# Optimization experiments

Hardware: AMD Instinct MI355X
Metric: run time of the kernel (lower is better)

## Reference

```python
import jax, jax.numpy as jnp
import numpy as np

B, N, K = 4, 40960, 16
D_IN, D_OUT = 32, 64


def setup_inputs() -> dict:
    key = jax.random.key(0)
    keys = iter(jax.random.split(key, 48))
    def nrm(shape, scale):
        return (jax.random.normal(next(keys), shape, jnp.float32) * scale).astype(jnp.float32)
    inp = {
        "feature": jax.random.normal(next(keys), (B, N, D_IN), jnp.float32),
        "xyz": jax.random.uniform(next(keys), (B, N, 3), jnp.float32),
        "neigh_idx": jax.random.randint(next(keys), (B, N, K), 0, N, jnp.int32),
    }
    def conv_bn(name, cin, cout):
        inp["w_" + name] = nrm((cin, cout), (2.0 / cin) ** 0.5)
        inp["s_" + name] = 1.0 + nrm((cout,), 0.1)  # folded BN scale: gamma/sqrt(var+eps)
        inp["b_" + name] = nrm((cout,), 0.1)        # folded BN bias: beta - mean*scale
    conv_bn("mlp1", D_IN, D_OUT // 2)
    conv_bn("lfa1", 10, D_OUT // 2)
    inp["w_att1_fc"] = nrm((D_OUT, D_OUT), (2.0 / D_OUT) ** 0.5)
    conv_bn("att1_mlp", D_OUT, D_OUT // 2)
    conv_bn("lfa2", D_OUT // 2, D_OUT // 2)
    inp["w_att2_fc"] = nrm((D_OUT, D_OUT), (2.0 / D_OUT) ** 0.5)
    conv_bn("att2_mlp", D_OUT, D_OUT)
    conv_bn("mlp2", D_OUT, 2 * D_OUT)
    conv_bn("sc", D_IN, 2 * D_OUT)
    return inp


def _gather(pc, idx):
    # pc: [B,N,D], idx: [B,N,K] -> [B,N,K,D]
    b, n, k = idx.shape
    flat = jnp.take_along_axis(pc, idx.reshape(b, n * k, 1), axis=1)
    return flat.reshape(b, n, k, pc.shape[-1])


def _cb(x, w, s, b, relu=True):
    # 1x1 conv + folded BN (+ ReLU), channels-last
    y = jnp.einsum('...i,io->...o', x, w) * s + b
    return jnp.maximum(y, 0.0) if relu else y


def _att_pool(fs, w_fc, w, s, b):
    # fs: [B,N,K,C]; softmax-attention pooling over K, then mlp
    scores = jax.nn.softmax(jnp.einsum('bnkc,cd->bnkd', fs, w_fc), axis=2)
    agg = jnp.sum(fs * scores, axis=2)  # [B,N,C]
    return _cb(agg, w, s, b)


def _rel_pos(xyz, idx):
    nbr = _gather(xyz, idx)                           # [B,N,K,3]
    tile = jnp.broadcast_to(xyz[:, :, None, :], nbr.shape)
    rel = tile - nbr
    dist = jnp.sqrt(jnp.sum(rel * rel, axis=-1, keepdims=True))
    return jnp.concatenate([dist, rel, tile, nbr], axis=-1)  # [B,N,K,10]


def reference(feature, xyz, neigh_idx,
              w_mlp1, s_mlp1, b_mlp1,
              w_lfa1, s_lfa1, b_lfa1,
              w_att1_fc, w_att1_mlp, s_att1_mlp, b_att1_mlp,
              w_lfa2, s_lfa2, b_lfa2,
              w_att2_fc, w_att2_mlp, s_att2_mlp, b_att2_mlp,
              w_mlp2, s_mlp2, b_mlp2,
              w_sc, s_sc, b_sc):
    f_pc = _cb(feature, w_mlp1, s_mlp1, b_mlp1)                   # [B,N,d/2]
    f_xyz = _cb(_rel_pos(xyz, neigh_idx), w_lfa1, s_lfa1, b_lfa1)  # [B,N,K,d/2]
    f_nb = _gather(f_pc, neigh_idx)                                # [B,N,K,d/2]
    f_agg = _att_pool(jnp.concatenate([f_nb, f_xyz], axis=-1),
                      w_att1_fc, w_att1_mlp, s_att1_mlp, b_att1_mlp)  # [B,N,d/2]
    f_xyz2 = _cb(f_xyz, w_lfa2, s_lfa2, b_lfa2)                    # [B,N,K,d/2]
    f_nb2 = _gather(f_agg, neigh_idx)                              # [B,N,K,d/2]
    f_pc2 = _att_pool(jnp.concatenate([f_nb2, f_xyz2], axis=-1),
                      w_att2_fc, w_att2_mlp, s_att2_mlp, b_att2_mlp)  # [B,N,d]
    out = _cb(f_pc2, w_mlp2, s_mlp2, b_mlp2, relu=False)           # [B,N,2d]
    sc = _cb(feature, w_sc, s_sc, b_sc, relu=False)
    return jax.nn.leaky_relu(out + sc, negative_slope=0.2)
```

## Files before the change

### kernel.cpp

```cpp
#include <hip/hip_runtime.h>
#include <hip/hip_bf16.h>

#define NPTS  40960
#define BNPTS 163840
#define KNB   16

#define PK_MLP1 0
#define PK_FC1  1280
#define PK_FC2  6912
#define PK_L1   12544
#define PK_L2   13824
#define PK_M1   15104
#define PK_M2   17920
#define PK_W2   23552
#define PK_WS   34816
#define PK_TOTAL 39936

using bf16x8 = __attribute__((ext_vector_type(8))) short;
using f32x4  = __attribute__((ext_vector_type(4))) float;

__device__ __forceinline__ unsigned short f2bf(float x) {
    union { float f; unsigned u; } v; v.f = x;
    unsigned r = v.u + 0x7fffu + ((v.u >> 16) & 1u);
    return (unsigned short)(r >> 16);
}
__device__ __forceinline__ float bf2f(unsigned short u) {
    union { unsigned u; float f; } v; v.u = ((unsigned)u) << 16;
    return v.f;
}
__device__ __forceinline__ unsigned pk2(float lo, float hi) {
    union { __hip_bfloat162 h; unsigned u; } v;
    v.h = __float22bfloat162_rn(float2{lo, hi});
    return v.u;
}
__device__ __forceinline__ bf16x8 pack8(float a0, float a1, float a2, float a3,
                                        float a4, float a5, float a6, float a7) {
    union { unsigned u[4]; bf16x8 v; } w;
    w.u[0] = pk2(a0, a1); w.u[1] = pk2(a2, a3);
    w.u[2] = pk2(a4, a5); w.u[3] = pk2(a6, a7);
    return w.v;
}
__device__ __forceinline__ f32x4 mfma16(bf16x8 a, bf16x8 b, f32x4 c) {
    return __builtin_amdgcn_mfma_f32_16x16x32_bf16(a, b, c, 0, 0, 0);
}
__device__ __forceinline__ float exp2_fast(float x) { return __builtin_amdgcn_exp2f(x); }
__device__ __forceinline__ float rcp_fast(float x)  { return __builtin_amdgcn_rcpf(x); }

__global__ __launch_bounds__(256)
void k_prep(const float* __restrict__ wm1, const float* __restrict__ wfc1,
            const float* __restrict__ wfc2,
            const float* __restrict__ wlfa1, const float* __restrict__ slfa1, const float* __restrict__ blfa1,
            const float* __restrict__ wlfa2,
            const float* __restrict__ wam1, const float* __restrict__ wam2,
            const float* __restrict__ w2, const float* __restrict__ wsc,
            unsigned short* __restrict__ pk)
{
    const int tid = threadIdx.x, blk = blockIdx.x;
    const float LOG2E = 1.4426950408889634f;
    switch (blk) {
    case 0:
        for (int t = tid; t < 32 * 32; t += 256) {
            int c = t >> 5, d = t & 31;
            int slot = (d & 1) * 16 + (d >> 1);
            pk[PK_MLP1 + slot * 40 + c] = f2bf(wm1[t]);
        }
        break;
    case 1:
        for (int t = tid; t < 64 * 64; t += 256) {
            int c = t >> 6, d = t & 63;
            pk[PK_FC1 + d * 88 + c] = f2bf(wfc1[t] * LOG2E);
        }
        break;
    case 2:
        for (int t = tid; t < 64 * 64; t += 256) {
            int c = t >> 6, d = t & 63;
            pk[PK_FC2 + d * 88 + c] = f2bf(wfc2[t] * LOG2E);
        }
        break;
    case 3:
        for (int t = tid; t < 32 * 32; t += 256) {
            int k = t >> 5, d = t & 31;
            int slot = (d & 1) * 16 + (d >> 1);
            float v1 = k < 10 ? wlfa1[k * 32 + d] * slfa1[d] : (k == 10 ? blfa1[d] : 0.f);
            pk[PK_L1 + slot * 40 + k] = f2bf(v1);
            pk[PK_L2 + slot * 40 + k] = f2bf(wlfa2[k * 32 + d]);
        }
        break;
    case 4:
        for (int t = tid; t < 64 * 32; t += 256) {
            int c = t / 32, d = t % 32;
            int slot = (d & 1) * 16 + (d >> 1);
            pk[PK_M1 + slot * 88 + c] = f2bf(wam1[t]);
        }
        break;
    case 5:
        for (int t = tid; t < 64 * 64; t += 256) {
            int c = t >> 6, d = t & 63;
            int slot = (d >> 5) * 32 + (d & 1) * 16 + ((d & 31) >> 1);
            pk[PK_M2 + slot * 88 + c] = f2bf(wam2[t]);
        }
        break;
    case 6:
        for (int t = tid; t < 64 * 128; t += 256) {
            int c = t >> 7, d = t & 127;
            int slot = (d >> 5) * 32 + (d & 1) * 16 + ((d & 31) >> 1);
            pk[PK_W2 + slot * 88 + c] = f2bf(w2[t]);
        }
        break;
    case 7:
        for (int t = tid; t < 32 * 128; t += 256) {
            int c = t >> 7, d = t & 127;
            int slot = (d >> 5) * 32 + (d & 1) * 16 + ((d & 31) >> 1);
            pk[PK_WS + slot * 40 + c] = f2bf(wsc[t]);
        }
        break;
    }
}

__global__ __launch_bounds__(256)
void k_mlp1(const float* __restrict__ feature, const unsigned short* __restrict__ pk,
            const float* __restrict__ s, const float* __restrict__ b,
            const float* __restrict__ xyz, float* __restrict__ xyz4,
            unsigned short* __restrict__ f_pc)
{
    const int tid = threadIdx.x;
    {
        int idx = blockIdx.x * 256 + tid;
        float3 v = *(const float3*)&xyz[(size_t)idx * 3];
        *(float4*)&xyz4[(size_t)idx * 4] = make_float4(v.x, v.y, v.z, 0.f);
    }
    const int lid = tid & 63, wv = tid >> 6;
    const int col = lid & 15, quad = lid >> 4;
    bf16x8 B0 = *(const bf16x8*)&pk[PK_MLP1 + col * 40 + quad * 8];
    bf16x8 B1 = *(const bf16x8*)&pk[PK_MLP1 + (16 + col) * 40 + quad * 8];
    float s0 = s[2 * col], b0 = b[2 * col], s1 = s[2 * col + 1], b1 = b[2 * col + 1];
    for (int itp = 0; itp < 4; itp++) {
        const int p0 = blockIdx.x * 256 + wv * 64 + itp * 16;
        const float* fr = &feature[(size_t)(p0 + col) * 32 + quad * 8];
        float4 u0 = *(const float4*)fr;
        float4 u1 = *(const float4*)(fr + 4);
        bf16x8 a = pack8(u0.x, u0.y, u0.z, u0.w, u1.x, u1.y, u1.z, u1.w);
        f32x4 z = {0.f, 0.f, 0.f, 0.f};
        f32x4 d0 = mfma16(a, B0, z);
        f32x4 d1 = mfma16(a, B1, z);
        #pragma unroll
        for (int r = 0; r < 4; r++) {
            int p = p0 + quad * 4 + r;
            float ye = fmaxf(d0[r] * s0 + b0, 0.f);
            float yo = fmaxf(d1[r] * s1 + b1, 0.f);
            *(unsigned*)&f_pc[(size_t)p * 32 + 2 * col] = pk2(ye, yo);
        }
    }
}

template<int NOUT, bool HAS_LFA2>
__global__ __launch_bounds__(256, 4)
void k_att(const float* __restrict__ xyz4, const int* __restrict__ nidx,
           const unsigned short* __restrict__ src,
           const unsigned short* __restrict__ wl1T, const unsigned short* __restrict__ wl2T,
           const float* __restrict__ slfa2, const float* __restrict__ blfa2,
           const unsigned short* __restrict__ wfcT, const unsigned short* __restrict__ wmT,
           const float* __restrict__ smlp, const float* __restrict__ bmlp,
           unsigned short* __restrict__ out)
{
    constexpr int NP = NOUT / 32;
    constexpr int WS = 88;
    __shared__ __align__(16) char smem[23552];
    char* uni = smem;

    const int tid = threadIdx.x;
    const int lid = tid & 63, wv = tid >> 6;
    const int col = lid & 15, quad = lid >> 4;

    bf16x8 Bfc[4][2];
    #pragma unroll
    for (int nt = 0; nt < 4; nt++)
        #pragma unroll
        for (int ks = 0; ks < 2; ks++)
            Bfc[nt][ks] = *(const bf16x8*)&wfcT[(nt * 16 + col) * WS + ks * 32 + quad * 8];
    bf16x8 Bl1e = *(const bf16x8*)&wl1T[col * 40 + quad * 8];
    bf16x8 Bl1o = *(const bf16x8*)&wl1T[(16 + col) * 40 + quad * 8];
    bf16x8 Bl2e{}, Bl2o{};
    float sl2e = 0.f, bl2e = 0.f, sl2o = 0.f, bl2o = 0.f;
    if (HAS_LFA2) {
        Bl2e = *(const bf16x8*)&wl2T[col * 40 + quad * 8];
        Bl2o = *(const bf16x8*)&wl2T[(16 + col) * 40 + quad * 8];
        sl2e = slfa2[2 * col]; bl2e = blfa2[2 * col];
        sl2o = slfa2[2 * col + 1]; bl2o = blfa2[2 * col + 1];
    }
    float sme[NP], bme[NP], smo[NP], bmo[NP];
    #pragma unroll
    for (int tp = 0; tp < NP; tp++) {
        sme[tp] = smlp[tp * 32 + 2 * col]; bme[tp] = bmlp[tp * 32 + 2 * col];
        smo[tp] = smlp[tp * 32 + 2 * col + 1]; bmo[tp] = bmlp[tp * 32 + 2 * col + 1];
    }

    unsigned short* fc  = (unsigned short*)(uni) + wv * 1408;
    unsigned short* ag  = (unsigned short*)(uni + 11264) + wv * 1152;
    unsigned short* nb  = (unsigned short*)(uni + 20480) + wv * 256;
    float*          cxy = (float*)(uni + 22528) + wv * 64;

    const int blk = (int)blockIdx.x;
    const int vblk = (blk & 7) * 320 + (blk >> 3);
    const int pbase = vblk * 64 + wv * 16;
    const int pb = (pbase / NPTS) * NPTS;
    const unsigned short* srcb = src + (size_t)pb * 32;
    const float4* x4  = (const float4*)xyz4;
    const float4* x4b = x4 + pb;

    {
        int4 t4 = *(const int4*)&nidx[(size_t)pbase * KNB + lid * 4];
        ushort4 u = make_ushort4((unsigned short)t4.x, (unsigned short)t4.y,
                                 (unsigned short)t4.z, (unsigned short)t4.w);
        *(ushort4*)&nb[lid * 4] = u;
        if (lid < 16) *(float4*)&cxy[lid * 4] = x4[pbase + lid];
    }

    const f32x4 z = {0.f, 0.f, 0.f, 0.f};
    bf16x8 vs; float nx = 0.f, ny = 0.f, nz = 0.f;
    {
        int j = (int)nb[col];
        vs = *(const bf16x8*)(srcb + (size_t)j * 32 + quad * 8);
        if (quad < 2) { float4 t = x4b[j]; nx = t.x; ny = t.y; nz = t.z; }
    }

    #pragma unroll 1
    for (int it = 0; it < 16; it++) {
        bf16x8 a0 = vs;
        *(bf16x8*)&fc[col * WS + quad * 8] = a0;

        float cx = cxy[it * 4], cy = cxy[it * 4 + 1], cz = cxy[it * 4 + 2];
        float rx = cx - nx, ry = cy - ny, rz = cz - nz;
        float dd = sqrtf(rx * rx + ry * ry + rz * rz);
        float f0 = 0.f, f1 = 0.f, f2 = 0.f, f3 = 0.f, f4 = 0.f, f5 = 0.f, f6 = 0.f, f7 = 0.f;
        if (quad == 0)      { f0 = dd; f1 = rx; f2 = ry; f3 = rz; f4 = cx; f5 = cy; f6 = cz; f7 = nx; }
        else if (quad == 1) { f0 = ny; f1 = nz; f2 = 1.0f; }
        bf16x8 al = pack8(f0, f1, f2, f3, f4, f5, f6, f7);

        {
            int itn = it < 15 ? it + 1 : 15;
            int j = (int)nb[itn * 16 + col];
            vs = *(const bf16x8*)(srcb + (size_t)j * 32 + quad * 8);
            if (quad < 2) { float4 t = x4b[j]; nx = t.x; ny = t.y; nz = t.z; }
        }

        {
            __builtin_amdgcn_s_setprio(1);
            f32x4 d0 = mfma16(al, Bl1e, z);
            f32x4 d1 = mfma16(al, Bl1o, z);
            __builtin_amdgcn_s_setprio(0);
            #pragma unroll
            for (int r = 0; r < 4; r++) {
                float ye = fmaxf(d0[r], 0.f);
                float yo = fmaxf(d1[r], 0.f);
                *(unsigned*)&fc[(quad * 4 + r) * WS + 32 + 2 * col] = pk2(ye, yo);
            }
            if (HAS_LFA2) {
                bf16x8 a2 = *(const bf16x8*)&fc[col * WS + 32 + quad * 8];
                __builtin_amdgcn_s_setprio(1);
                f32x4 e0 = mfma16(a2, Bl2e, z);
                f32x4 e1 = mfma16(a2, Bl2o, z);
                __builtin_amdgcn_s_setprio(0);
                #pragma unroll
                for (int r = 0; r < 4; r++) {
                    float ye = fmaxf(e0[r] * sl2e + bl2e, 0.f);
                    float yo = fmaxf(e1[r] * sl2o + bl2o, 0.f);
                    *(unsigned*)&fc[(quad * 4 + r) * WS + 32 + 2 * col] = pk2(ye, yo);
                }
            }
        }

        {
            bf16x8 a1 = *(const bf16x8*)&fc[col * WS + 32 + quad * 8];
            #pragma unroll
            for (int nt = 0; nt < 4; nt++) {
                __builtin_amdgcn_s_setprio(1);
                f32x4 L = mfma16(a1, Bfc[nt][1], mfma16(a0, Bfc[nt][0], z));
                __builtin_amdgcn_s_setprio(0);
                float e0 = exp2_fast(L[0]), e1 = exp2_fast(L[1]);
                float e2 = exp2_fast(L[2]), e3 = exp2_fast(L[3]);
                float sden = (e0 + e1) + (e2 + e3);
                const unsigned short* frr = &fc[quad * 4 * WS + nt * 16 + col];
                float av = e0 * bf2f(frr[0]) + e1 * bf2f(frr[WS]) + e2 * bf2f(frr[2 * WS]) + e3 * bf2f(frr[3 * WS]);
                av   += __shfl_xor(av, 16, 64);
                sden += __shfl_xor(sden, 16, 64);
                av   += __shfl_xor(av, 32, 64);
                sden += __shfl_xor(sden, 32, 64);
                if (quad == 0) ag[it * 72 + nt * 16 + col] = f2bf(av * rcp_fast(sden));
            }
        }
    }

    {
        bf16x8 am0 = *(const bf16x8*)&ag[col * 72 + quad * 8];
        bf16x8 am1 = *(const bf16x8*)&ag[col * 72 + 32 + quad * 8];
        #pragma unroll
        for (int tp = 0; tp < NP; tp++) {
            bf16x8 Be0, Be1, Bo0, Bo1;
            if constexpr (NOUT == 32) {
                Be0 = *(const bf16x8*)&wmT[col * WS + quad * 8];
                Be1 = *(const bf16x8*)&wmT[col * WS + 32 + quad * 8];
                Bo0 = *(const bf16x8*)&wmT[(16 + col) * WS + quad * 8];
                Bo1 = *(const bf16x8*)&wmT[(16 + col) * WS + 32 + quad * 8];
            } else {
                Be0 = *(const bf16x8*)&wmT[(tp * 32 + col) * WS + quad * 8];
                Be1 = *(const bf16x8*)&wmT[(tp * 32 + col) * WS + 32 + quad * 8];
                Bo0 = *(const bf16x8*)&wmT[(tp * 32 + 16 + col) * WS + quad * 8];
                Bo1 = *(const bf16x8*)&wmT[(tp * 32 + 16 + col) * WS + 32 + quad * 8];
            }
            __builtin_amdgcn_s_setprio(1);
            f32x4 de = mfma16(am1, Be1, mfma16(am0, Be0, z));
            f32x4 dq = mfma16(am1, Bo1, mfma16(am0, Bo0, z));
            __builtin_amdgcn_s_setprio(0);
            #pragma unroll
            for (int r = 0; r < 4; r++) {
                int pp = pbase + quad * 4 + r;
                float ye = fmaxf(de[r] * sme[tp] + bme[tp], 0.f);
                float yo = fmaxf(dq[r] * smo[tp] + bmo[tp], 0.f);
                *(unsigned*)&out[(size_t)pp * NOUT + tp * 32 + 2 * col] = pk2(ye, yo);
            }
        }
    }
}

__global__ __launch_bounds__(256)
void k_out(const unsigned short* __restrict__ f_pc2, const float* __restrict__ feature,
           const unsigned short* __restrict__ pk,
           const float* __restrict__ s2, const float* __restrict__ b2,
           const float* __restrict__ ssc, const float* __restrict__ bsc,
           float* __restrict__ out)
{
    const int tid = threadIdx.x;
    const int lid = tid & 63, wv = tid >> 6;
    const int col = lid & 15, quad = lid >> 4;
    const unsigned short* w2T = pk + PK_W2;
    const unsigned short* wsT = pk + PK_WS;
    float sse[4], sso[4], ste[4], sto[4], bbe[4], bbo[4];
    #pragma unroll
    for (int m = 0; m < 4; m++) {
        int ce = m * 32 + 2 * col, co = ce + 1;
        sse[m] = s2[ce]; sso[m] = s2[co];
        ste[m] = ssc[ce]; sto[m] = ssc[co];
        bbe[m] = b2[ce] + bsc[ce]; bbo[m] = b2[co] + bsc[co];
    }
    const f32x4 z = {0.f, 0.f, 0.f, 0.f};
    #pragma unroll 1
    for (int itp = 0; itp < 2; itp++) {
        const int p0 = blockIdx.x * 128 + wv * 32 + itp * 16;
        const unsigned short* ar = &f_pc2[(size_t)(p0 + col) * 64 + quad * 8];
        bf16x8 a10 = *(const bf16x8*)ar;
        bf16x8 a11 = *(const bf16x8*)(ar + 32);
        const float* fr = &feature[(size_t)(p0 + col) * 32 + quad * 8];
        float4 u0 = *(const float4*)fr;
        float4 u1 = *(const float4*)(fr + 4);
        bf16x8 a2 = pack8(u0.x, u0.y, u0.z, u0.w, u1.x, u1.y, u1.z, u1.w);
        #pragma unroll
        for (int m = 0; m < 4; m++) {
            bf16x8 ke0 = *(const bf16x8*)&w2T[(m * 32 + col) * 88 + quad * 8];
            bf16x8 ke1 = *(const bf16x8*)&w2T[(m * 32 + col) * 88 + 32 + quad * 8];
            bf16x8 ko0 = *(const bf16x8*)&w2T[(m * 32 + 16 + col) * 88 + quad * 8];
            bf16x8 ko1 = *(const bf16x8*)&w2T[(m * 32 + 16 + col) * 88 + 32 + quad * 8];
            bf16x8 se  = *(const bf16x8*)&wsT[(m * 32 + col) * 40 + quad * 8];
            bf16x8 so  = *(const bf16x8*)&wsT[(m * 32 + 16 + col) * 40 + quad * 8];
            f32x4 de = mfma16(a11, ke1, mfma16(a10, ke0, z));
            f32x4 dq = mfma16(a11, ko1, mfma16(a10, ko0, z));
            f32x4 ee = mfma16(a2, se, z);
            f32x4 eo = mfma16(a2, so, z);
            #pragma unroll
            for (int r = 0; r < 4; r++) {
                float ye = de[r] * sse[m] + ee[r] * ste[m] + bbe[m];
                float yo = dq[r] * sso[m] + eo[r] * sto[m] + bbo[m];
                ye = ye > 0.f ? ye : 0.2f * ye;
                yo = yo > 0.f ? yo : 0.2f * yo;
                *(float2*)&out[(size_t)(p0 + quad * 4 + r) * 128 + m * 32 + 2 * col] =
                    make_float2(ye, yo);
            }
        }
    }
}

extern "C" void kernel_launch(void* const* d_in, const int* in_sizes, int n_in,
                              void* d_out, int out_size, void* d_ws, size_t ws_size,
                              hipStream_t stream) {
    const float* feature = (const float*)d_in[0];
    const float* xyz     = (const float*)d_in[1];
    const int*   nidx    = (const int*)d_in[2];
    const float* w_mlp1 = (const float*)d_in[3];
    const float* s_mlp1 = (const float*)d_in[4];
    const float* b_mlp1 = (const float*)d_in[5];
    const float* w_lfa1 = (const float*)d_in[6];
    const float* s_lfa1 = (const float*)d_in[7];
    const float* b_lfa1 = (const float*)d_in[8];
    const float* w_att1_fc  = (const float*)d_in[9];
    const float* w_att1_mlp = (const float*)d_in[10];
    const float* s_att1_mlp = (const float*)d_in[11];
    const float* b_att1_mlp = (const float*)d_in[12];
    const float* w_lfa2 = (const float*)d_in[13];
    const float* s_lfa2 = (const float*)d_in[14];
    const float* b_lfa2 = (const float*)d_in[15];
    const float* w_att2_fc  = (const float*)d_in[16];
    const float* w_att2_mlp = (const float*)d_in[17];
    const float* s_att2_mlp = (const float*)d_in[18];
    const float* b_att2_mlp = (const float*)d_in[19];
    const float* w_mlp2 = (const float*)d_in[20];
    const float* s_mlp2 = (const float*)d_in[21];
    const float* b_mlp2 = (const float*)d_in[22];
    const float* w_sc = (const float*)d_in[23];
    const float* s_sc = (const float*)d_in[24];
    const float* b_sc = (const float*)d_in[25];

    unsigned short* f_pc  = (unsigned short*)d_ws;
    unsigned short* f_agg = f_pc  + (size_t)BNPTS * 32;
    unsigned short* f_pc2 = f_agg + (size_t)BNPTS * 32;
    unsigned short* pkw   = f_pc2 + (size_t)BNPTS * 64;
    float*          xyz4  = (float*)(pkw + PK_TOTAL);
    float* out = (float*)d_out;

    k_prep<<<8, 256, 0, stream>>>(
        w_mlp1, w_att1_fc, w_att2_fc,
        w_lfa1, s_lfa1, b_lfa1, w_lfa2,
        w_att1_mlp, w_att2_mlp, w_mlp2, w_sc, pkw);
    k_mlp1<<<BNPTS / 256, 256, 0, stream>>>(feature, pkw, s_mlp1, b_mlp1, xyz, xyz4, f_pc);
    k_att<32, false><<<BNPTS / 64, 256, 0, stream>>>(
        xyz4, nidx, f_pc,
        pkw + PK_L1, pkw + PK_L1,
        s_lfa1, b_lfa1,
        pkw + PK_FC1, pkw + PK_M1, s_att1_mlp, b_att1_mlp, f_agg);
    k_att<64, true><<<BNPTS / 64, 256, 0, stream>>>(
        xyz4, nidx, f_agg,
        pkw + PK_L1, pkw + PK_L2,
        s_lfa2, b_lfa2,
        pkw + PK_FC2, pkw + PK_M2, s_att2_mlp, b_att2_mlp, f_pc2);
    k_out<<<BNPTS / 128, 256, 0, stream>>>(
        f_pc2, feature, pkw,
        s_mlp2, b_mlp2, s_sc, b_sc, out);
}
```

Measured before the change: 355.5 us.

## Fuse output MLP and shortcut into second attention kernel; drop setprio hints

The final mlp2 + shortcut + leaky-ReLU stage is folded into the tail of the second attention kernel. Each wave now stages its f_pc2 tile in a new per-wave LDS buffer and runs the output matmuls directly from it, so the separate k_out launch and the global round trip of f_pc2 go away. The s_setprio hints around the MFMA calls are also removed. In exchange the second attention kernel uses more LDS and registers, which may reduce occupancy.

Result: faster. 337.3 us (-5.1%).

```diff
diff --git a/kernel.cpp b/kernel.cpp
--- a/kernel.cpp
+++ b/kernel.cpp
@@ -161,11 +161,17 @@
            const float* __restrict__ slfa2, const float* __restrict__ blfa2,
            const unsigned short* __restrict__ wfcT, const unsigned short* __restrict__ wmT,
            const float* __restrict__ smlp, const float* __restrict__ bmlp,
-           unsigned short* __restrict__ out)
+           unsigned short* __restrict__ out,
+           const float* __restrict__ feature,
+           const unsigned short* __restrict__ w2T, const unsigned short* __restrict__ wsT,
+           const float* __restrict__ s2, const float* __restrict__ b2,
+           const float* __restrict__ ssc, const float* __restrict__ bsc,
+           float* __restrict__ outF)
 {
     constexpr int NP = NOUT / 32;
     constexpr int WS = 88;
     __shared__ __align__(16) char smem[23552];
+    __shared__ __align__(16) unsigned short fp2_s[NOUT == 64 ? 4 * 1152 : 8];
     char* uni = smem;
 
     const int tid = threadIdx.x;
@@ -199,6 +205,7 @@
     unsigned short* ag  = (unsigned short*)(uni + 11264) + wv * 1152;
     unsigned short* nb  = (unsigned short*)(uni + 20480) + wv * 256;
     float*          cxy = (float*)(uni + 22528) + wv * 64;
+    unsigned short* fp2 = fp2_s + wv * 1152;
 
     const int blk = (int)blockIdx.x;
     const int vblk = (blk & 7) * 320 + (blk >> 3);
@@ -245,10 +252,8 @@
         }
 
         {
-            __builtin_amdgcn_s_setprio(1);
             f32x4 d0 = mfma16(al, Bl1e, z);
             f32x4 d1 = mfma16(al, Bl1o, z);
-            __builtin_amdgcn_s_setprio(0);
             #pragma unroll
             for (int r = 0; r < 4; r++) {
                 float ye = fmaxf(d0[r], 0.f);
@@ -257,10 +262,8 @@
             }
             if (HAS_LFA2) {
                 bf16x8 a2 = *(const bf16x8*)&fc[col * WS + 32 + quad * 8];
-                __builtin_amdgcn_s_setprio(1);
                 f32x4 e0 = mfma16(a2, Bl2e, z);
                 f32x4 e1 = mfma16(a2, Bl2o, z);
-                __builtin_amdgcn_s_setprio(0);
                 #pragma unroll
                 for (int r = 0; r < 4; r++) {
                     float ye = fmaxf(e0[r] * sl2e + bl2e, 0.f);
@@ -274,9 +277,7 @@
             bf16x8 a1 = *(const bf16x8*)&fc[col * WS + 32 + quad * 8];
             #pragma unroll
             for (int nt = 0; nt < 4; nt++) {
-                __builtin_amdgcn_s_setprio(1);
                 f32x4 L = mfma16(a1, Bfc[nt][1], mfma16(a0, Bfc[nt][0], z));
-                __builtin_amdgcn_s_setprio(0);
                 float e0 = exp2_fast(L[0]), e1 = exp2_fast(L[1]);
                 float e2 = exp2_fast(L[2]), e3 = exp2_fast(L[3]);
                 float sden = (e0 + e1) + (e2 + e3);
@@ -308,49 +309,26 @@
                 Bo0 = *(const bf16x8*)&wmT[(tp * 32 + 16 + col) * WS + quad * 8];
                 Bo1 = *(const bf16x8*)&wmT[(tp * 32 + 16 + col) * WS + 32 + quad * 8];
             }
-            __builtin_amdgcn_s_setprio(1);
             f32x4 de = mfma16(am1, Be1, mfma16(am0, Be0, z));
             f32x4 dq = mfma16(am1, Bo1, mfma16(am0, Bo0, z));
-            __builtin_amdgcn_s_setprio(0);
             #pragma unroll
             for (int r = 0; r < 4; r++) {
-                int pp = pbase + quad * 4 + r;
                 float ye = fmaxf(de[r] * sme[tp] + bme[tp], 0.f);
                 float yo = fmaxf(dq[r] * smo[tp] + bmo[tp], 0.f);
-                *(unsigned*)&out[(size_t)pp * NOUT + tp * 32 + 2 * col] = pk2(ye, yo);
-            }
-        }
-    }
-}
-
-__global__ __launch_bounds__(256)
-void k_out(const unsigned short* __restrict__ f_pc2, const float* __restrict__ feature,
-           const unsigned short* __restrict__ pk,
-           const float* __restrict__ s2, const float* __restrict__ b2,
-           const float* __restrict__ ssc, const float* __restrict__ bsc,
-           float* __restrict__ out)
-{
-    const int tid = threadIdx.x;
-    const int lid = tid & 63, wv = tid >> 6;
-    const int col = lid & 15, quad = lid >> 4;
-    const unsigned short* w2T = pk + PK_W2;
-    const unsigned short* wsT = pk + PK_WS;
-    float sse[4], sso[4], ste[4], sto[4], bbe[4], bbo[4];
-    #pragma unroll
-    for (int m = 0; m < 4; m++) {
-        int ce = m * 32 + 2 * col, co = ce + 1;
-        sse[m] = s2[ce]; sso[m] = s2[co];
-        ste[m] = ssc[ce]; sto[m] = ssc[co];
-        bbe[m] = b2[ce] + bsc[ce]; bbo[m] = b2[co] + bsc[co];
-    }
-    const f32x4 z = {0.f, 0.f, 0.f, 0.f};
-    #pragma unroll 1
-    for (int itp = 0; itp < 2; itp++) {
-        const int p0 = blockIdx.x * 128 + wv * 32 + itp * 16;
-        const unsigned short* ar = &f_pc2[(size_t)(p0 + col) * 64 + quad * 8];
-        bf16x8 a10 = *(const bf16x8*)ar;
-        bf16x8 a11 = *(const bf16x8*)(ar + 32);
-        const float* fr = &feature[(size_t)(p0 + col) * 32 + quad * 8];
+                if constexpr (NOUT == 64) {
+                    *(unsigned*)&fp2[(quad * 4 + r) * 72 + tp * 32 + 2 * col] = pk2(ye, yo);
+                } else {
+                    int pp = pbase + quad * 4 + r;
+                    *(unsigned*)&out[(size_t)pp * NOUT + tp * 32 + 2 * col] = pk2(ye, yo);
+                }
+            }
+        }
+    }
+
+    if constexpr (NOUT == 64) {
+        bf16x8 a10 = *(const bf16x8*)&fp2[col * 72 + quad * 8];
+        bf16x8 a11 = *(const bf16x8*)&fp2[col * 72 + 32 + quad * 8];
+        const float* fr = &feature[(size_t)(pbase + col) * 32 + quad * 8];
         float4 u0 = *(const float4*)fr;
         float4 u1 = *(const float4*)(fr + 4);
         bf16x8 a2 = pack8(u0.x, u0.y, u0.z, u0.w, u1.x, u1.y, u1.z, u1.w);
@@ -366,13 +344,17 @@
             f32x4 dq = mfma16(a11, ko1, mfma16(a10, ko0, z));
             f32x4 ee = mfma16(a2, se, z);
             f32x4 eo = mfma16(a2, so, z);
+            int ce = m * 32 + 2 * col, co = ce + 1;
+            float sse = s2[ce], sso = s2[co];
+            float ste = ssc[ce], sto = ssc[co];
+            float bbe = b2[ce] + bsc[ce], bbo = b2[co] + bsc[co];
             #pragma unroll
             for (int r = 0; r < 4; r++) {
-                float ye = de[r] * sse[m] + ee[r] * ste[m] + bbe[m];
-                float yo = dq[r] * sso[m] + eo[r] * sto[m] + bbo[m];
+                float ye = de[r] * sse + ee[r] * ste + bbe;
+                float yo = dq[r] * sso + eo[r] * sto + bbo;
                 ye = ye > 0.f ? ye : 0.2f * ye;
                 yo = yo > 0.f ? yo : 0.2f * yo;
-                *(float2*)&out[(size_t)(p0 + quad * 4 + r) * 128 + m * 32 + 2 * col] =
+                *(float2*)&outF[(size_t)(pbase + quad * 4 + r) * 128 + m * 32 + 2 * col] =
                     make_float2(ye, yo);
             }
         }
@@ -425,13 +407,14 @@
         xyz4, nidx, f_pc,
         pkw + PK_L1, pkw + PK_L1,
         s_lfa1, b_lfa1,
-        pkw + PK_FC1, pkw + PK_M1, s_att1_mlp, b_att1_mlp, f_agg);
+        pkw + PK_FC1, pkw + PK_M1, s_att1_mlp, b_att1_mlp, f_agg,
+        feature, pkw + PK_W2, pkw + PK_WS,
+        s_mlp2, b_mlp2, s_sc, b_sc, out);
     k_att<64, true><<<BNPTS / 64, 256, 0, stream>>>(
         xyz4, nidx, f_agg,
         pkw + PK_L1, pkw + PK_L2,
         s_lfa2, b_lfa2,
-        pkw + PK_FC2, pkw + PK_M2, s_att2_mlp, b_att2_mlp, f_pc2);
-    k_out<<<BNPTS / 128, 256, 0, stream>>>(
-        f_pc2, feature, pkw,
+        pkw + PK_FC2, pkw + PK_M2, s_att2_mlp, b_att2_mlp, f_pc2,
+        feature, pkw + PK_W2, pkw + PK_WS,
         s_mlp2, b_mlp2, s_sc, b_sc, out);
 }
```
